# Kernel tuning notes

Measured on AMD Instinct MI355X. Metric: run time of the kernel, lower is better.

## Reference

```python
import jax, jax.numpy as jnp
import numpy as np

N_NODES = 100000
N_EDGES = 1600000
IN_CH = 128
HEADS = 4
OUT_CH = 32


def setup_inputs() -> dict:
    key = jax.random.key(0)
    k = jax.random.split(key, 6)
    x = jax.random.normal(k[0], (N_NODES, IN_CH), dtype=jnp.float32)
    edge_index = jax.random.randint(k[1], (2, N_EDGES), 0, N_NODES, dtype=jnp.int64)
    edge_weight = jax.random.uniform(k[2], (N_EDGES,), dtype=jnp.float32)
    # torch Linear weight layout: (out_features, in_features) = (heads*out_ch, in_ch)
    W = jax.random.normal(k[3], (HEADS * OUT_CH, IN_CH), dtype=jnp.float32) * (1.0 / np.sqrt(IN_CH))
    a_src = jax.random.normal(k[4], (1, HEADS, OUT_CH), dtype=jnp.float32) * 0.1
    a_dst = jax.random.normal(k[5], (1, HEADS, OUT_CH), dtype=jnp.float32) * 0.1
    return {"x": x, "edge_index": edge_index, "edge_weight": edge_weight,
            "W": W, "a_src": a_src, "a_dst": a_dst}


def reference(x, edge_index, edge_weight, W, a_src, a_dst):
    N = x.shape[0]
    H, C = a_src.shape[1], a_src.shape[2]
    # linear projection then reshape to (N, H, C)
    h = (x @ W.T).reshape(N, H, C)
    src, dst = edge_index[0], edge_index[1]
    # per-node attention logits (node-level, then gathered -> same math as
    # (h[src]*a_src).sum(-1), computed once per node instead of per edge)
    s_src = jnp.sum(h * a_src, axis=-1)  # (N, H)
    s_dst = jnp.sum(h * a_dst, axis=-1)  # (N, H)
    alpha = jax.nn.leaky_relu(s_src[src] + s_dst[dst], negative_slope=0.2)  # (E, H)
    alpha = alpha * edge_weight[:, None]
    # segment softmax over dst; torch scatter_reduce amax with include_self=True
    # includes the zero init, so max is taken vs. 0 via zeros init
    amax = jnp.zeros((N, H), dtype=alpha.dtype).at[dst].max(alpha)
    alpha = jnp.exp(alpha - amax[dst])
    asum = jnp.zeros((N, H), dtype=alpha.dtype).at[dst].add(alpha)
    alpha = alpha / (asum[dst] + 1e-8)  # (E, H)
    # weighted scatter-add aggregation
    out = jnp.zeros((N, H, C), dtype=h.dtype).at[dst].add(h[src] * alpha[:, :, None])
    # concat=True
    return out.reshape(N, H * C)
```

## Files before the change

kernel.cpp:

```cpp
#include <hip/hip_runtime.h>

#define N_NODES 100000
#define N_EDGES 1600000
#define NBKT 391
#define BKT_SLACK 5120
#define EPB 4096
#define BINA_BLOCKS ((N_EDGES + EPB - 1) / EPB)

typedef __attribute__((ext_vector_type(8))) short short8;
typedef __attribute__((ext_vector_type(4))) float f32x4;

__device__ __forceinline__ unsigned short f2bf(float f) {
    unsigned u = __float_as_uint(f);
    u = u + 0x7fffu + ((u >> 16) & 1u);
    return (unsigned short)(u >> 16);
}
__device__ __forceinline__ float bf2f(unsigned short h) {
    return __uint_as_float((unsigned)h << 16);
}

__global__ __launch_bounds__(256) void wsplit_kernel(
    const float* __restrict__ W, unsigned short* __restrict__ Wh,
    unsigned short* __restrict__ Wl)
{
    int i = blockIdx.x * 256 + threadIdx.x;
    float v = W[i];
    unsigned short hi = f2bf(v);
    Wh[i] = hi;
    Wl[i] = f2bf(v - bf2f(hi));
}

__global__ __launch_bounds__(256) void proj_kernel(
    const float* __restrict__ x, const unsigned short* __restrict__ Whg,
    const unsigned short* __restrict__ Wlg,
    const float* __restrict__ a_src, const float* __restrict__ a_dst,
    unsigned short* __restrict__ hout, float* __restrict__ s_src,
    float* __restrict__ s_dst)
{
    __shared__ char smem[81920];
    char* Wh = smem;
    char* Wl = smem + 32768;
    char* xh = smem + 65536;
    char* xl = smem + 73728;
    const int t = threadIdx.x;
    const int br = blockIdx.x * 32;

    {
        int o = t >> 1, kh = (t & 1) * 64;
#pragma unroll
        for (int i = 0; i < 16; ++i) {
            int k = kh + i * 4;
            int byt = o * 256 + (((k >> 3) ^ (o & 7)) * 16) + (k & 7) * 2;
            *(ushort4*)(Wh + byt) = *(const ushort4*)&Whg[o * 128 + k];
            *(ushort4*)(Wl + byt) = *(const ushort4*)&Wlg[o * 128 + k];
        }
    }
    {
        int row = t >> 3;
        size_t gb = (size_t)(br + row) * 128;
#pragma unroll
        for (int i = 0; i < 4; ++i) {
            int k = ((t & 7) * 4 + i) * 4;
            float4 v = *(const float4*)&x[gb + k];
            ushort4 hi, lo;
            hi.x = f2bf(v.x); lo.x = f2bf(v.x - bf2f(hi.x));
            hi.y = f2bf(v.y); lo.y = f2bf(v.y - bf2f(hi.y));
            hi.z = f2bf(v.z); lo.z = f2bf(v.z - bf2f(hi.z));
            hi.w = f2bf(v.w); lo.w = f2bf(v.w - bf2f(hi.w));
            int byt = row * 256 + (((k >> 3) ^ (row & 7)) * 16) + (k & 7) * 2;
            *(ushort4*)(xh + byt) = hi;
            *(ushort4*)(xl + byt) = lo;
        }
    }
    __syncthreads();

    const int wave = t >> 6, lane = t & 63;
    const int lr = lane & 15, q = lane >> 4;
    f32x4 acc[2][2] = {};

#pragma unroll
    for (int ks = 0; ks < 4; ++ks) {
        int sl = ((ks * 4 + q) ^ (lr & 7)) * 16;
        int a0o = lr * 256 + sl, a1o = (16 + lr) * 256 + sl;
        int b0o = (wave * 32 + lr) * 256 + sl, b1o = (wave * 32 + 16 + lr) * 256 + sl;
        short8 ah0 = *(const short8*)(xh + a0o);
        short8 ah1 = *(const short8*)(xh + a1o);
        short8 al0 = *(const short8*)(xl + a0o);
        short8 al1 = *(const short8*)(xl + a1o);
        short8 bh0 = *(const short8*)(Wh + b0o);
        short8 bh1 = *(const short8*)(Wh + b1o);
        short8 bl0 = *(const short8*)(Wl + b0o);
        short8 bl1 = *(const short8*)(Wl + b1o);
        acc[0][0] = __builtin_amdgcn_mfma_f32_16x16x32_bf16(ah0, bh0, acc[0][0], 0, 0, 0);
        acc[0][1] = __builtin_amdgcn_mfma_f32_16x16x32_bf16(ah0, bh1, acc[0][1], 0, 0, 0);
        acc[1][0] = __builtin_amdgcn_mfma_f32_16x16x32_bf16(ah1, bh0, acc[1][0], 0, 0, 0);
        acc[1][1] = __builtin_amdgcn_mfma_f32_16x16x32_bf16(ah1, bh1, acc[1][1], 0, 0, 0);
        acc[0][0] = __builtin_amdgcn_mfma_f32_16x16x32_bf16(al0, bh0, acc[0][0], 0, 0, 0);
        acc[0][1] = __builtin_amdgcn_mfma_f32_16x16x32_bf16(al0, bh1, acc[0][1], 0, 0, 0);
        acc[1][0] = __builtin_amdgcn_mfma_f32_16x16x32_bf16(al1, bh0, acc[1][0], 0, 0, 0);
        acc[1][1] = __builtin_amdgcn_mfma_f32_16x16x32_bf16(al1, bh1, acc[1][1], 0, 0, 0);
        acc[0][0] = __builtin_amdgcn_mfma_f32_16x16x32_bf16(ah0, bl0, acc[0][0], 0, 0, 0);
        acc[0][1] = __builtin_amdgcn_mfma_f32_16x16x32_bf16(ah0, bl1, acc[0][1], 0, 0, 0);
        acc[1][0] = __builtin_amdgcn_mfma_f32_16x16x32_bf16(ah1, bl0, acc[1][0], 0, 0, 0);
        acc[1][1] = __builtin_amdgcn_mfma_f32_16x16x32_bf16(ah1, bl1, acc[1][1], 0, 0, 0);
    }

    float as0 = a_src[wave * 32 + lr], as1 = a_src[wave * 32 + 16 + lr];
    float ad0 = a_dst[wave * 32 + lr], ad1 = a_dst[wave * 32 + 16 + lr];
#pragma unroll
    for (int r = 0; r < 2; ++r) {
#pragma unroll
        for (int reg = 0; reg < 4; ++reg) {
            float ps = acc[r][0][reg] * as0 + acc[r][1][reg] * as1;
            float pd = acc[r][0][reg] * ad0 + acc[r][1][reg] * ad1;
            ps += __shfl_xor(ps, 1); ps += __shfl_xor(ps, 2);
            ps += __shfl_xor(ps, 4); ps += __shfl_xor(ps, 8);
            pd += __shfl_xor(pd, 1); pd += __shfl_xor(pd, 2);
            pd += __shfl_xor(pd, 4); pd += __shfl_xor(pd, 8);
            if (lr == 0) {
                int grow = br + r * 16 + q * 4 + reg;
                s_src[grow * 4 + wave] = ps;
                s_dst[grow * 4 + wave] = pd;
            }
        }
    }

    __syncthreads();
    unsigned short* hl = (unsigned short*)xh;
#pragma unroll
    for (int r = 0; r < 2; ++r)
#pragma unroll
        for (int c = 0; c < 2; ++c)
#pragma unroll
            for (int reg = 0; reg < 4; ++reg)
                hl[(r * 16 + q * 4 + reg) * 128 + wave * 32 + c * 16 + lr] =
                    f2bf(acc[r][c][reg]);
    __syncthreads();
    {
        int row = t >> 3, cb = (t & 7) * 16;
        uint4 v0 = *(uint4*)&hl[row * 128 + cb];
        uint4 v1 = *(uint4*)&hl[row * 128 + cb + 8];
        *(uint4*)&hout[(size_t)(br + row) * 128 + cb] = v0;
        *(uint4*)&hout[(size_t)(br + row) * 128 + cb + 8] = v1;
    }
}

__global__ __launch_bounds__(256) void binA_kernel(
    const int* __restrict__ ei, const float* __restrict__ ew,
    int* __restrict__ gcur, uint2* __restrict__ ebin)
{
    __shared__ int hist[NBKT];
    __shared__ int runbase[NBKT];
    const int t = threadIdx.x;
    const int base = blockIdx.x * EPB;
    for (int b = t; b < NBKT; b += 256) hist[b] = 0;
    __syncthreads();
#pragma unroll
    for (int i = 0; i < EPB / 256; ++i) {
        int e = base + i * 256 + t;
        if (e < N_EDGES) atomicAdd(&hist[ei[N_EDGES + e] >> 8], 1);
    }
    __syncthreads();
    for (int b = t; b < NBKT; b += 256) {
        int c = hist[b];
        runbase[b] = (c > 0) ? atomicAdd(&gcur[b], c) : 0;
        hist[b] = 0;
    }
    __syncthreads();
#pragma unroll
    for (int i = 0; i < EPB / 256; ++i) {
        int e = base + i * 256 + t;
        if (e >= N_EDGES) continue;
        int s = ei[e];
        int d = ei[N_EDGES + e];
        int b = d >> 8;
        int lpos = atomicAdd(&hist[b], 1);
        ebin[(size_t)b * BKT_SLACK + runbase[b] + lpos] =
            make_uint2((unsigned)s | ((unsigned)(d & 255) << 17),
                       __float_as_uint(ew[e]));
    }
}

__global__ __launch_bounds__(512) void bscan_kernel(
    const int* __restrict__ gcur, int* __restrict__ bktbase)
{
    __shared__ int sh[512];
    int t = threadIdx.x;
    int v = (t < NBKT) ? gcur[t] : 0;
    sh[t] = v; __syncthreads();
    for (int off = 1; off < 512; off <<= 1) {
        int a = sh[t];
        int b = (t >= off) ? sh[t - off] : 0;
        __syncthreads();
        sh[t] = a + b;
        __syncthreads();
    }
    if (t < NBKT) bktbase[t] = sh[t] - v;
}

__global__ __launch_bounds__(256) void binB_kernel(
    const uint2* __restrict__ ebin, const int* __restrict__ gcur,
    const int* __restrict__ bktbase, uint2* __restrict__ earr,
    int* __restrict__ rowp, int* __restrict__ deg)
{
    __shared__ int cnt[256];
    __shared__ int sc[256];
    __shared__ int cur[256];
    const int b = blockIdx.x;
    const int t = threadIdx.x;
    cnt[t] = 0;
    __syncthreads();
    const int count = gcur[b];
    const uint2* bp = ebin + (size_t)b * BKT_SLACK;
    for (int i = t; i < count; i += 256)
        atomicAdd(&cnt[(bp[i].x >> 17) & 255], 1);
    __syncthreads();
    int c = cnt[t];
    sc[t] = c; __syncthreads();
    for (int off = 1; off < 256; off <<= 1) {
        int a = sc[t];
        int bb = (t >= off) ? sc[t - off] : 0;
        __syncthreads();
        sc[t] = a + bb;
        __syncthreads();
    }
    int excl = sc[t] - c;
    int base = bktbase[b];
    int node = b * 256 + t;
    if (node < N_NODES) { rowp[node] = base + excl; deg[node] = c; }
    cur[t] = base + excl;
    __syncthreads();
    for (int i = t; i < count; i += 256) {
        uint2 rec = bp[i];
        int pos = atomicAdd(&cur[(rec.x >> 17) & 255], 1);
        earr[pos] = make_uint2(rec.x & 0x1FFFFu, rec.y);
    }
}

__global__ __launch_bounds__(256) void gather_kernel(
    const uint2* __restrict__ earr, const int* __restrict__ rowp,
    const int* __restrict__ deg, const float* __restrict__ s_src,
    const float* __restrict__ s_dst,
    const unsigned short* __restrict__ hbuf, float* __restrict__ out)
{
    __shared__ float lds_alpha[4][64][4];
    __shared__ int lds_src[4][64];
    const int w = threadIdx.x >> 6;
    const int lane = threadIdx.x & 63;
    const int n = blockIdx.x * 4 + w;
    const int start = rowp[n];
    const int dg = deg[n];
    const float4 sd = *(const float4*)&s_dst[n * 4];
    const int half = lane >> 5;
    const int cl = lane & 31;
    const int hd2 = cl >> 3;

    float ps0 = 0.f, ps1 = 0.f, ps2 = 0.f, ps3 = 0.f;
    float ac0 = 0.f, ac1 = 0.f, ac2 = 0.f, ac3 = 0.f;

    for (int b0 = 0; b0 < dg; b0 += 64) {
        int nb = dg - b0; if (nb > 64) nb = 64;
        float a0 = 0.f, a1 = 0.f, a2 = 0.f, a3 = 0.f;
        int sid = 0;
        if (lane < nb) {
            uint2 rec = earr[start + b0 + lane];
            sid = (int)rec.x;
            float wgt = __uint_as_float(rec.y);
            float4 ss = *(const float4*)&s_src[sid * 4];
            float v;
            v = ss.x + sd.x; v = (v > 0.f ? v : 0.2f * v) * wgt; a0 = __expf(v);
            v = ss.y + sd.y; v = (v > 0.f ? v : 0.2f * v) * wgt; a1 = __expf(v);
            v = ss.z + sd.z; v = (v > 0.f ? v : 0.2f * v) * wgt; a2 = __expf(v);
            v = ss.w + sd.w; v = (v > 0.f ? v : 0.2f * v) * wgt; a3 = __expf(v);
            ps0 += a0; ps1 += a1; ps2 += a2; ps3 += a3;
        }
        *(float4*)&lds_alpha[w][lane][0] = make_float4(a0, a1, a2, a3);
        lds_src[w][lane] = sid;

        int nb8 = (nb + 7) & ~7;
        for (int i = 0; i < nb8; i += 8) {
#pragma unroll
            for (int j = 0; j < 4; ++j) {
                int e = i + j * 2 + half;
                float coef = lds_alpha[w][e][hd2];
                int s = lds_src[w][e];
                uint2 hv = *(const uint2*)&hbuf[(size_t)s * 128 + cl * 4];
                ac0 = fmaf(coef, __uint_as_float(hv.x << 16), ac0);
                ac1 = fmaf(coef, __uint_as_float(hv.x & 0xffff0000u), ac1);
                ac2 = fmaf(coef, __uint_as_float(hv.y << 16), ac2);
                ac3 = fmaf(coef, __uint_as_float(hv.y & 0xffff0000u), ac3);
            }
        }
    }
    ac0 += __shfl_xor(ac0, 32);
    ac1 += __shfl_xor(ac1, 32);
    ac2 += __shfl_xor(ac2, 32);
    ac3 += __shfl_xor(ac3, 32);
#pragma unroll
    for (int off = 1; off < 64; off <<= 1) {
        ps0 += __shfl_xor(ps0, off);
        ps1 += __shfl_xor(ps1, off);
        ps2 += __shfl_xor(ps2, off);
        ps3 += __shfl_xor(ps3, off);
    }
    float sv = (hd2 & 2) ? ((hd2 & 1) ? ps3 : ps2) : ((hd2 & 1) ? ps1 : ps0);
    float inv = 1.f / (sv + 1e-8f);
    if (lane < 32) {
        float4 o = {ac0 * inv, ac1 * inv, ac2 * inv, ac3 * inv};
        *(float4*)&out[(size_t)n * 128 + cl * 4] = o;
    }
}

extern "C" void kernel_launch(void* const* d_in, const int* in_sizes, int n_in,
                              void* d_out, int out_size, void* d_ws, size_t ws_size,
                              hipStream_t stream)
{
    const float* x     = (const float*)d_in[0];
    const int*   ei    = (const int*)d_in[1];
    const float* ew    = (const float*)d_in[2];
    const float* W     = (const float*)d_in[3];
    const float* a_src = (const float*)d_in[4];
    const float* a_dst = (const float*)d_in[5];
    float* out = (float*)d_out;
    char* ws = (char*)d_ws;

    unsigned short* hbuf = (unsigned short*)(ws);
    float* s_src = (float*)(ws + 25600000);
    float* s_dst = (float*)(ws + 27200000);
    int*   deg     = (int*)(ws + 28800000);
    int*   rowp    = (int*)(ws + 29200000);
    int*   gcur    = (int*)(ws + 29600000);
    int*   bktbase = (int*)(ws + 29602048);
    unsigned short* Whg = (unsigned short*)(ws + 29604096);
    unsigned short* Wlg = (unsigned short*)(ws + 29636864);
    uint2* earr  = (uint2*)(ws + 29669632);
    uint2* ebin  = (uint2*)(ws + 42469632);

    hipMemsetAsync(gcur, 0, 2048, stream);

    wsplit_kernel<<<64, 256, 0, stream>>>(W, Whg, Wlg);
    proj_kernel<<<N_NODES / 32, 256, 0, stream>>>(x, Whg, Wlg, a_src, a_dst,
                                                  hbuf, s_src, s_dst);
    binA_kernel<<<BINA_BLOCKS, 256, 0, stream>>>(ei, ew, gcur, ebin);
    bscan_kernel<<<1, 512, 0, stream>>>(gcur, bktbase);
    binB_kernel<<<NBKT, 256, 0, stream>>>(ebin, gcur, bktbase, earr, rowp, deg);
    gather_kernel<<<N_NODES / 4, 256, 0, stream>>>(earr, rowp, deg, s_src, s_dst,
                                                   hbuf, out);
}
```

Baseline: 179.2 us.

## Fuse weight split and bucket scan into consumers; use 16 lanes per node in gather

Removes the separate W bf16 split kernel by splitting W inside each projection block, and removes the single-block bucket scan by having each binB block sum the preceding bucket counts itself. The gather kernel now maps 16 lanes to a node (16 nodes per block) with 8 channels per lane via 16-byte loads, instead of a full wavefront per node. This cuts two launches and the idle lanes for low-degree nodes, in exchange for redundant W conversion in every projection block, redundant prefix sums in binB, and lower per-node memory parallelism.

```diff
diff --git a/kernel.cpp b/kernel.cpp
--- a/kernel.cpp
+++ b/kernel.cpp
@@ -19,20 +19,8 @@
     return __uint_as_float((unsigned)h << 16);
 }
 
-__global__ __launch_bounds__(256) void wsplit_kernel(
-    const float* __restrict__ W, unsigned short* __restrict__ Wh,
-    unsigned short* __restrict__ Wl)
-{
-    int i = blockIdx.x * 256 + threadIdx.x;
-    float v = W[i];
-    unsigned short hi = f2bf(v);
-    Wh[i] = hi;
-    Wl[i] = f2bf(v - bf2f(hi));
-}
-
 __global__ __launch_bounds__(256) void proj_kernel(
-    const float* __restrict__ x, const unsigned short* __restrict__ Whg,
-    const unsigned short* __restrict__ Wlg,
+    const float* __restrict__ x, const float* __restrict__ W,
     const float* __restrict__ a_src, const float* __restrict__ a_dst,
     unsigned short* __restrict__ hout, float* __restrict__ s_src,
     float* __restrict__ s_dst)
@@ -50,9 +38,15 @@
 #pragma unroll
         for (int i = 0; i < 16; ++i) {
             int k = kh + i * 4;
+            float4 v = *(const float4*)&W[o * 128 + k];
+            ushort4 hi, lo;
+            hi.x = f2bf(v.x); lo.x = f2bf(v.x - bf2f(hi.x));
+            hi.y = f2bf(v.y); lo.y = f2bf(v.y - bf2f(hi.y));
+            hi.z = f2bf(v.z); lo.z = f2bf(v.z - bf2f(hi.z));
+            hi.w = f2bf(v.w); lo.w = f2bf(v.w - bf2f(hi.w));
             int byt = o * 256 + (((k >> 3) ^ (o & 7)) * 16) + (k & 7) * 2;
-            *(ushort4*)(Wh + byt) = *(const ushort4*)&Whg[o * 128 + k];
-            *(ushort4*)(Wl + byt) = *(const ushort4*)&Wlg[o * 128 + k];
+            *(ushort4*)(Wh + byt) = hi;
+            *(ushort4*)(Wl + byt) = lo;
         }
     }
     {
@@ -181,33 +175,27 @@
     }
 }
 
-__global__ __launch_bounds__(512) void bscan_kernel(
-    const int* __restrict__ gcur, int* __restrict__ bktbase)
-{
-    __shared__ int sh[512];
-    int t = threadIdx.x;
-    int v = (t < NBKT) ? gcur[t] : 0;
-    sh[t] = v; __syncthreads();
-    for (int off = 1; off < 512; off <<= 1) {
-        int a = sh[t];
-        int b = (t >= off) ? sh[t - off] : 0;
-        __syncthreads();
-        sh[t] = a + b;
-        __syncthreads();
-    }
-    if (t < NBKT) bktbase[t] = sh[t] - v;
-}
-
 __global__ __launch_bounds__(256) void binB_kernel(
     const uint2* __restrict__ ebin, const int* __restrict__ gcur,
-    const int* __restrict__ bktbase, uint2* __restrict__ earr,
-    int* __restrict__ rowp, int* __restrict__ deg)
+    uint2* __restrict__ earr, int* __restrict__ rowp, int* __restrict__ deg)
 {
     __shared__ int cnt[256];
     __shared__ int sc[256];
     __shared__ int cur[256];
     const int b = blockIdx.x;
     const int t = threadIdx.x;
+    int acc = 0;
+    for (int i = t; i < b; i += 256) acc += gcur[i];
+    sc[t] = acc; __syncthreads();
+    for (int off = 1; off < 256; off <<= 1) {
+        int a = sc[t];
+        int bb = (t >= off) ? sc[t - off] : 0;
+        __syncthreads();
+        sc[t] = a + bb;
+        __syncthreads();
+    }
+    const int base = sc[255];
+    __syncthreads();
     cnt[t] = 0;
     __syncthreads();
     const int count = gcur[b];
@@ -225,7 +213,6 @@
         __syncthreads();
     }
     int excl = sc[t] - c;
-    int base = bktbase[b];
     int node = b * 256 + t;
     if (node < N_NODES) { rowp[node] = base + excl; deg[node] = c; }
     cur[t] = base + excl;
@@ -243,27 +230,26 @@
     const float* __restrict__ s_dst,
     const unsigned short* __restrict__ hbuf, float* __restrict__ out)
 {
-    __shared__ float lds_alpha[4][64][4];
-    __shared__ int lds_src[4][64];
-    const int w = threadIdx.x >> 6;
-    const int lane = threadIdx.x & 63;
-    const int n = blockIdx.x * 4 + w;
+    __shared__ float lds_alpha[16][16][4];
+    __shared__ int lds_src[16][16];
+    const int ln = threadIdx.x >> 4;
+    const int sub = threadIdx.x & 15;
+    const int n = blockIdx.x * 16 + ln;
     const int start = rowp[n];
     const int dg = deg[n];
     const float4 sd = *(const float4*)&s_dst[n * 4];
-    const int half = lane >> 5;
-    const int cl = lane & 31;
-    const int hd2 = cl >> 3;
+    const int hd3 = sub >> 2;
 
     float ps0 = 0.f, ps1 = 0.f, ps2 = 0.f, ps3 = 0.f;
     float ac0 = 0.f, ac1 = 0.f, ac2 = 0.f, ac3 = 0.f;
-
-    for (int b0 = 0; b0 < dg; b0 += 64) {
-        int nb = dg - b0; if (nb > 64) nb = 64;
+    float ac4 = 0.f, ac5 = 0.f, ac6 = 0.f, ac7 = 0.f;
+
+    for (int b0 = 0; b0 < dg; b0 += 16) {
+        int nb = dg - b0; if (nb > 16) nb = 16;
         float a0 = 0.f, a1 = 0.f, a2 = 0.f, a3 = 0.f;
         int sid = 0;
-        if (lane < nb) {
-            uint2 rec = earr[start + b0 + lane];
+        if (sub < nb) {
+            uint2 rec = earr[start + b0 + sub];
             sid = (int)rec.x;
             float wgt = __uint_as_float(rec.y);
             float4 ss = *(const float4*)&s_src[sid * 4];
@@ -274,41 +260,37 @@
             v = ss.w + sd.w; v = (v > 0.f ? v : 0.2f * v) * wgt; a3 = __expf(v);
             ps0 += a0; ps1 += a1; ps2 += a2; ps3 += a3;
         }
-        *(float4*)&lds_alpha[w][lane][0] = make_float4(a0, a1, a2, a3);
-        lds_src[w][lane] = sid;
-
-        int nb8 = (nb + 7) & ~7;
-        for (int i = 0; i < nb8; i += 8) {
-#pragma unroll
-            for (int j = 0; j < 4; ++j) {
-                int e = i + j * 2 + half;
-                float coef = lds_alpha[w][e][hd2];
-                int s = lds_src[w][e];
-                uint2 hv = *(const uint2*)&hbuf[(size_t)s * 128 + cl * 4];
-                ac0 = fmaf(coef, __uint_as_float(hv.x << 16), ac0);
-                ac1 = fmaf(coef, __uint_as_float(hv.x & 0xffff0000u), ac1);
-                ac2 = fmaf(coef, __uint_as_float(hv.y << 16), ac2);
-                ac3 = fmaf(coef, __uint_as_float(hv.y & 0xffff0000u), ac3);
-            }
-        }
-    }
-    ac0 += __shfl_xor(ac0, 32);
-    ac1 += __shfl_xor(ac1, 32);
-    ac2 += __shfl_xor(ac2, 32);
-    ac3 += __shfl_xor(ac3, 32);
-#pragma unroll
-    for (int off = 1; off < 64; off <<= 1) {
+        *(float4*)&lds_alpha[ln][sub][0] = make_float4(a0, a1, a2, a3);
+        lds_src[ln][sub] = sid;
+
+#pragma unroll 2
+        for (int e = 0; e < nb; ++e) {
+            float coef = lds_alpha[ln][e][hd3];
+            int s = lds_src[ln][e];
+            uint4 hv = *(const uint4*)&hbuf[(size_t)s * 128 + sub * 8];
+            ac0 = fmaf(coef, __uint_as_float(hv.x << 16), ac0);
+            ac1 = fmaf(coef, __uint_as_float(hv.x & 0xffff0000u), ac1);
+            ac2 = fmaf(coef, __uint_as_float(hv.y << 16), ac2);
+            ac3 = fmaf(coef, __uint_as_float(hv.y & 0xffff0000u), ac3);
+            ac4 = fmaf(coef, __uint_as_float(hv.z << 16), ac4);
+            ac5 = fmaf(coef, __uint_as_float(hv.z & 0xffff0000u), ac5);
+            ac6 = fmaf(coef, __uint_as_float(hv.w << 16), ac6);
+            ac7 = fmaf(coef, __uint_as_float(hv.w & 0xffff0000u), ac7);
+        }
+    }
+#pragma unroll
+    for (int off = 1; off < 16; off <<= 1) {
         ps0 += __shfl_xor(ps0, off);
         ps1 += __shfl_xor(ps1, off);
         ps2 += __shfl_xor(ps2, off);
         ps3 += __shfl_xor(ps3, off);
     }
-    float sv = (hd2 & 2) ? ((hd2 & 1) ? ps3 : ps2) : ((hd2 & 1) ? ps1 : ps0);
+    float sv = (hd3 & 2) ? ((hd3 & 1) ? ps3 : ps2) : ((hd3 & 1) ? ps1 : ps0);
     float inv = 1.f / (sv + 1e-8f);
-    if (lane < 32) {
-        float4 o = {ac0 * inv, ac1 * inv, ac2 * inv, ac3 * inv};
-        *(float4*)&out[(size_t)n * 128 + cl * 4] = o;
-    }
+    float4 o0 = {ac0 * inv, ac1 * inv, ac2 * inv, ac3 * inv};
+    float4 o1 = {ac4 * inv, ac5 * inv, ac6 * inv, ac7 * inv};
+    *(float4*)&out[(size_t)n * 128 + sub * 8] = o0;
+    *(float4*)&out[(size_t)n * 128 + sub * 8 + 4] = o1;
 }
 
 extern "C" void kernel_launch(void* const* d_in, const int* in_sizes, int n_in,
@@ -327,23 +309,18 @@
     unsigned short* hbuf = (unsigned short*)(ws);
     float* s_src = (float*)(ws + 25600000);
     float* s_dst = (float*)(ws + 27200000);
-    int*   deg     = (int*)(ws + 28800000);
-    int*   rowp    = (int*)(ws + 29200000);
-    int*   gcur    = (int*)(ws + 29600000);
-    int*   bktbase = (int*)(ws + 29602048);
-    unsigned short* Whg = (unsigned short*)(ws + 29604096);
-    unsigned short* Wlg = (unsigned short*)(ws + 29636864);
+    int*   deg   = (int*)(ws + 28800000);
+    int*   rowp  = (int*)(ws + 29200000);
+    int*   gcur  = (int*)(ws + 29600000);
     uint2* earr  = (uint2*)(ws + 29669632);
     uint2* ebin  = (uint2*)(ws + 42469632);
 
     hipMemsetAsync(gcur, 0, 2048, stream);
 
-    wsplit_kernel<<<64, 256, 0, stream>>>(W, Whg, Wlg);
-    proj_kernel<<<N_NODES / 32, 256, 0, stream>>>(x, Whg, Wlg, a_src, a_dst,
+    proj_kernel<<<N_NODES / 32, 256, 0, stream>>>(x, W, a_src, a_dst,
                                                   hbuf, s_src, s_dst);
     binA_kernel<<<BINA_BLOCKS, 256, 0, stream>>>(ei, ew, gcur, ebin);
-    bscan_kernel<<<1, 512, 0, stream>>>(gcur, bktbase);
-    binB_kernel<<<NBKT, 256, 0, stream>>>(ebin, gcur, bktbase, earr, rowp, deg);
-    gather_kernel<<<N_NODES / 4, 256, 0, stream>>>(earr, rowp, deg, s_src, s_dst,
-                                                   hbuf, out);
-}
+    binB_kernel<<<NBKT, 256, 0, stream>>>(ebin, gcur, earr, rowp, deg);
+    gather_kernel<<<N_NODES / 16, 256, 0, stream>>>(earr, rowp, deg, s_src, s_dst,
+                                                    hbuf, out);
+}
```

Result: no change. 179.8 us (+0.4%).
